# Kernel optimization log

Measured on AMD Instinct MI355X. Metric: run time of the kernel, lower is better.

## Reference

```python
import jax, jax.numpy as jnp
import numpy as np

EMBED_DIM = 1024
NUM_HEADS = 16
HEAD_DIM = EMBED_DIM // NUM_HEADS


def setup_inputs() -> dict:
    key = jax.random.key(0)
    ks = jax.random.split(key, 6)
    B, S = 2, 2048
    x = jax.random.normal(ks[0], (B, S, EMBED_DIM), dtype=jnp.float32)
    # causal boolean mask, broadcast to (B, H, S, S)
    causal = jnp.tril(jnp.ones((S, S), dtype=bool))
    mask = jnp.broadcast_to(causal, (B, NUM_HEADS, S, S))
    s_in = 1.0 / np.sqrt(EMBED_DIM)
    qkv_w = jax.random.normal(ks[1], (3 * EMBED_DIM, EMBED_DIM), dtype=jnp.float32) * s_in
    qkv_b = jax.random.normal(ks[2], (3 * EMBED_DIM,), dtype=jnp.float32) * 0.01
    proj_w = jax.random.normal(ks[3], (EMBED_DIM, EMBED_DIM), dtype=jnp.float32) * s_in
    proj_b = jax.random.normal(ks[4], (EMBED_DIM,), dtype=jnp.float32) * 0.01
    return {"x": x, "mask": mask, "qkv_w": qkv_w, "qkv_b": qkv_b,
            "proj_w": proj_w, "proj_b": proj_b}


def reference(x, mask, qkv_w, qkv_b, proj_w, proj_b):
    B, S, E = x.shape
    H, D = NUM_HEADS, HEAD_DIM
    qkv = x @ qkv_w.T + qkv_b                     # (B, S, 3E)
    q, k, v = jnp.split(qkv, 3, axis=-1)
    # (B, H, S, D)
    q = q.reshape(B, S, H, D).transpose(0, 2, 1, 3)
    k = k.reshape(B, S, H, D).transpose(0, 2, 1, 3)
    v = v.reshape(B, S, H, D).transpose(0, 2, 1, 3)
    scale = D ** (-0.5)
    attn = jnp.einsum('bhqd,bhkd->bhqk', q, k) * scale
    attn = jnp.where(mask, attn, jnp.float32(-10000.0))
    attn = attn - jnp.max(attn, axis=-1, keepdims=True)
    attn = jax.nn.softmax(attn, axis=-1)
    attn = jnp.where(mask, attn, jnp.float32(0.0))
    # dropout is identity in eval mode
    out = jnp.einsum('bhqk,bhkd->bhqd', attn, v)
    out = out.transpose(0, 2, 1, 3).reshape(B, S, E)
    return out @ proj_w.T + proj_b
```

## Files before the change

kernel.cpp:

```cpp
#include <hip/hip_runtime.h>
#include <hip/hip_bf16.h>

#define BATCH 2
#define SEQ 2048
#define EMBED 1024
#define NHEADS 16
#define HDIM 64

typedef __hip_bfloat16 bf16;
typedef __attribute__((ext_vector_type(8))) short bf16x8;
typedef __attribute__((ext_vector_type(4))) short bf16x4;
typedef __attribute__((ext_vector_type(4))) float f32x4;

typedef const __attribute__((address_space(1))) void* gaddr_t;
typedef __attribute__((address_space(3))) void* laddr_t;

__device__ __forceinline__ bf16x8 lds_frag8(const bf16* p) {
    const bf16x4 a = *(const bf16x4*)p;
    const bf16x4 b = *(const bf16x4*)(p + 4);
    return __builtin_shufflevector(a, b, 0, 1, 2, 3, 4, 5, 6, 7);
}

__global__ __launch_bounds__(256)
void f2b_kernel(const float* __restrict__ in, bf16* __restrict__ out, int n4)
{
    const int i = blockIdx.x * 256 + threadIdx.x;
    if (i >= n4) return;
    const float4 v = ((const float4*)in)[i];
    union { ushort4 u4; bf16 h[4]; } o;
    o.h[0] = __float2bfloat16(v.x);
    o.h[1] = __float2bfloat16(v.y);
    o.h[2] = __float2bfloat16(v.z);
    o.h[3] = __float2bfloat16(v.w);
    ((ushort4*)out)[i] = o.u4;
}

template<int MODE>
__global__ __launch_bounds__(256)
void gemm_bt(const bf16* __restrict__ A, const bf16* __restrict__ B,
             const float* __restrict__ bias, void* __restrict__ Cv,
             int M, int N, int K)
{
    __shared__ __align__(16) bf16 lA[128 * 32];
    __shared__ __align__(16) bf16 lB[128 * 32];
    const int tid  = threadIdx.x;
    const int bn   = blockIdx.x, bm = blockIdx.y;
    const int wave = tid >> 6, lane = tid & 63;
    const int wm   = (wave >> 1) << 6, wn = (wave & 1) << 6;
    const int quad = lane >> 4, l16 = lane & 15;

    f32x4 acc[4][4] = {};

    for (int kt = 0; kt < K; kt += 32) {
        __syncthreads();
        #pragma unroll
        for (int i = 0; i < 2; ++i) {
            const int c = tid + (i << 8);
            const int r = c >> 2, kc = (c & 3) << 3;
            const bf16* gA = A + (long)(bm * 128 + r) * K + (kt + kc);
            const bf16* gB = B + (long)(bn * 128 + r) * K + (kt + kc);
            __builtin_amdgcn_global_load_lds((gaddr_t)gA, (laddr_t)&lA[c << 3], 16, 0, 0);
            __builtin_amdgcn_global_load_lds((gaddr_t)gB, (laddr_t)&lB[c << 3], 16, 0, 0);
        }
        __syncthreads();

        bf16x8 af[4], bfr[4];
        #pragma unroll
        for (int t = 0; t < 4; ++t) {
            af[t]  = *(const bf16x8*)&lA[(wm + t * 16 + l16) * 32 + quad * 8];
            bfr[t] = *(const bf16x8*)&lB[(wn + t * 16 + l16) * 32 + quad * 8];
        }
        #pragma unroll
        for (int tm = 0; tm < 4; ++tm)
            #pragma unroll
            for (int tn = 0; tn < 4; ++tn)
                acc[tm][tn] = __builtin_amdgcn_mfma_f32_16x16x32_bf16(
                    af[tm], bfr[tn], acc[tm][tn], 0, 0, 0);
    }

    #pragma unroll
    for (int tm = 0; tm < 4; ++tm) {
        #pragma unroll
        for (int tn = 0; tn < 4; ++tn) {
            const int gn = bn * 128 + wn + tn * 16 + l16;
            const float bv = bias[gn];
            #pragma unroll
            for (int r = 0; r < 4; ++r) {
                const int gm = bm * 128 + wm + tm * 16 + quad * 4 + r;
                const float v = acc[tm][tn][r] + bv;
                if (MODE == 0) {
                    ((float*)Cv)[(long)gm * N + gn] = v;
                } else {
                    const int b = gm >> 11, s = gm & (SEQ - 1);
                    const int part = gn >> 10, h = (gn >> 6) & (NHEADS - 1), d = gn & (HDIM - 1);
                    const long off = ((((long)part * BATCH + b) * NHEADS + h) * SEQ + s) * HDIM + d;
                    ((bf16*)Cv)[off] = __float2bfloat16(v);
                }
            }
        }
    }
}

__global__ __launch_bounds__(256)
void attn_mfma(const bf16* __restrict__ Q, const bf16* __restrict__ K,
               const bf16* __restrict__ V, bf16* __restrict__ O)
{
    __shared__ __align__(16) bf16 kS[64 * 68];
    __shared__ __align__(16) bf16 vS[64 * 68];
    __shared__ __align__(16) bf16 pS[4 * 32 * 68];

    const int tid  = threadIdx.x;
    const int wave = tid >> 6, lane = tid & 63;
    const int quad = lane >> 4, l15 = lane & 15;
    const int qt   = (gridDim.x - 1) - blockIdx.x;
    const int bh   = blockIdx.y;
    const int q0   = qt * 128, qw0 = q0 + wave * 32;

    const bf16* Qb = Q + (long)bh * SEQ * HDIM;
    const bf16* Kb = K + (long)bh * SEQ * HDIM;
    const bf16* Vb = V + (long)bh * SEQ * HDIM;
    const short* vSs = (const short*)vS;
    bf16* pW = pS + wave * 32 * 68;

    bf16x8 qf[2][2];
    #pragma unroll
    for (int mt = 0; mt < 2; ++mt)
        #pragma unroll
        for (int c = 0; c < 2; ++c) {
            union { int4 i; bf16x8 v; } u;
            u.i = *(const int4*)(Qb + (long)(qw0 + mt * 16 + l15) * HDIM + c * 32 + quad * 8);
            qf[mt][c] = u.v;
        }

    f32x4 acc[2][4] = {};
    float lsum[8] = {};

    const int nkt = 2 * qt + 2;
    const float sc = 0.125f * 1.44269504088896340736f;

    for (int t = 0; t < nkt; ++t) {
        const int kb = t * 64;
        __syncthreads();
        #pragma unroll
        for (int i = 0; i < 2; ++i) {
            const int c = tid + (i << 8);
            const int row = c >> 3, col = (c & 7) << 3;
            const int4 kk = *(const int4*)(Kb + (long)(kb + row) * HDIM + col);
            const int4 vv = *(const int4*)(Vb + (long)(kb + row) * HDIM + col);
            *(int2*)&kS[row * 68 + col]     = make_int2(kk.x, kk.y);
            *(int2*)&kS[row * 68 + col + 4] = make_int2(kk.z, kk.w);
            *(int2*)&vS[row * 68 + col]     = make_int2(vv.x, vv.y);
            *(int2*)&vS[row * 68 + col + 4] = make_int2(vv.z, vv.w);
        }
        __syncthreads();
        if (kb > qw0 + 31) continue;

        f32x4 s[2][4] = {};
        #pragma unroll
        for (int c = 0; c < 2; ++c) {
            bf16x8 kf[4];
            #pragma unroll
            for (int nt = 0; nt < 4; ++nt)
                kf[nt] = lds_frag8(&kS[(nt * 16 + l15) * 68 + c * 32 + quad * 8]);
            #pragma unroll
            for (int mt = 0; mt < 2; ++mt)
                #pragma unroll
                for (int nt = 0; nt < 4; ++nt)
                    s[mt][nt] = __builtin_amdgcn_mfma_f32_16x16x32_bf16(
                        qf[mt][c], kf[nt], s[mt][nt], 0, 0, 0);
        }

        #pragma unroll
        for (int mt = 0; mt < 2; ++mt)
            #pragma unroll
            for (int nt = 0; nt < 4; ++nt)
                #pragma unroll
                for (int r = 0; r < 4; ++r) {
                    const int rl = mt * 16 + quad * 4 + r;
                    const int cl = nt * 16 + l15;
                    const float p = ((kb + cl) <= (qw0 + rl))
                        ? __builtin_amdgcn_exp2f(s[mt][nt][r] * sc) : 0.f;
                    lsum[mt * 4 + r] += p;
                    pW[rl * 68 + cl] = __float2bfloat16(p);
                }

        #pragma unroll
        for (int c = 0; c < 2; ++c) {
            bf16x8 pf[2];
            #pragma unroll
            for (int mt = 0; mt < 2; ++mt)
                pf[mt] = lds_frag8(&pW[(mt * 16 + l15) * 68 + c * 32 + quad * 8]);
            #pragma unroll
            for (int nt = 0; nt < 4; ++nt) {
                bf16x8 vf;
                #pragma unroll
                for (int j = 0; j < 8; ++j)
                    vf[j] = vSs[(c * 32 + quad * 8 + j) * 68 + nt * 16 + l15];
                #pragma unroll
                for (int mt = 0; mt < 2; ++mt)
                    acc[mt][nt] = __builtin_amdgcn_mfma_f32_16x16x32_bf16(
                        pf[mt], vf, acc[mt][nt], 0, 0, 0);
            }
        }
    }

    #pragma unroll
    for (int i = 0; i < 8; ++i) {
        #pragma unroll
        for (int m = 1; m < 16; m <<= 1) lsum[i] += __shfl_xor(lsum[i], m, 64);
        lsum[i] = 1.f / lsum[i];
    }

    const int b = bh >> 4, h = bh & 15;
    #pragma unroll
    for (int mt = 0; mt < 2; ++mt)
        #pragma unroll
        for (int r = 0; r < 4; ++r) {
            const int rl = mt * 16 + quad * 4 + r;
            bf16* orow = O + ((long)b * SEQ + (qw0 + rl)) * EMBED + h * HDIM;
            const float inv = lsum[mt * 4 + r];
            #pragma unroll
            for (int nt = 0; nt < 4; ++nt)
                orow[nt * 16 + l15] = __float2bfloat16(acc[mt][nt][r] * inv);
        }
}

extern "C" void kernel_launch(void* const* d_in, const int* in_sizes, int n_in,
                              void* d_out, int out_size, void* d_ws, size_t ws_size,
                              hipStream_t stream)
{
    const float* x      = (const float*)d_in[0];
    const float* qkv_w  = (const float*)d_in[2];
    const float* qkv_b  = (const float*)d_in[3];
    const float* proj_w = (const float*)d_in[4];
    const float* proj_b = (const float*)d_in[5];
    float* out = (float*)d_out;

    const long nX  = (long)BATCH * SEQ * EMBED;
    const long nQW = 3L * EMBED * EMBED;
    const long nPW = (long)EMBED * EMBED;
    const long per = (long)BATCH * NHEADS * SEQ * HDIM;

    bf16* xw  = (bf16*)d_ws;
    bf16* qwm = xw + nX;
    bf16* pwm = qwm + nQW;
    bf16* qw  = pwm + nPW;
    bf16* kw  = qw + per;
    bf16* vw  = kw + per;
    bf16* att = vw + per;

    f2b_kernel<<<(int)(nX  / 4 / 256), 256, 0, stream>>>(x,      xw,  (int)(nX  / 4));
    f2b_kernel<<<(int)(nQW / 4 / 256), 256, 0, stream>>>(qkv_w,  qwm, (int)(nQW / 4));
    f2b_kernel<<<(int)(nPW / 4 / 256), 256, 0, stream>>>(proj_w, pwm, (int)(nPW / 4));

    gemm_bt<1><<<dim3(3 * EMBED / 128, BATCH * SEQ / 128), 256, 0, stream>>>(
        xw, qwm, qkv_b, qw, BATCH * SEQ, 3 * EMBED, EMBED);

    attn_mfma<<<dim3(SEQ / 128, BATCH * NHEADS), 256, 0, stream>>>(qw, kw, vw, att);

    gemm_bt<0><<<dim3(EMBED / 128, BATCH * SEQ / 128), 256, 0, stream>>>(
        att, pwm, proj_b, out, BATCH * SEQ, EMBED, EMBED);
}
```

Baseline: 756.0 us.

## Split attention KV range across two blocks and combine partials; fuse conversions

The attention kernel now splits each query tile's key tiles into even and odd halves handled by separate blocks. Each block writes unnormalized fp32 partial outputs and row sums, and a new combine kernel adds the two halves, normalizes, and writes bf16. The change doubles the number of attention blocks on the GPU (512 to 1024). Because no running max is used, the halves can be summed directly. The three fp32-to-bf16 conversion launches are merged into one, and the V tile in LDS is padded to a stride of 70 to change bank access patterns. In exchange it adds fp32 partial-output traffic (about 33 MB written and read) and one extra launch.

```diff
diff --git a/kernel.cpp b/kernel.cpp
--- a/kernel.cpp
+++ b/kernel.cpp
@@ -22,17 +22,23 @@
 }
 
 __global__ __launch_bounds__(256)
-void f2b_kernel(const float* __restrict__ in, bf16* __restrict__ out, int n4)
-{
-    const int i = blockIdx.x * 256 + threadIdx.x;
-    if (i >= n4) return;
-    const float4 v = ((const float4*)in)[i];
+void f2b_all(const float* __restrict__ s0, bf16* __restrict__ d0, int n0,
+             const float* __restrict__ s1, bf16* __restrict__ d1, int n1,
+             const float* __restrict__ s2, bf16* __restrict__ d2, int n2)
+{
+    int i = blockIdx.x * 256 + threadIdx.x;
+    const float* s; bf16* d;
+    if (i < n0)                { s = s0; d = d0; }
+    else if ((i -= n0) < n1)   { s = s1; d = d1; }
+    else if ((i -= n1) < n2)   { s = s2; d = d2; }
+    else return;
+    const float4 v = ((const float4*)s)[i];
     union { ushort4 u4; bf16 h[4]; } o;
     o.h[0] = __float2bfloat16(v.x);
     o.h[1] = __float2bfloat16(v.y);
     o.h[2] = __float2bfloat16(v.z);
     o.h[3] = __float2bfloat16(v.w);
-    ((ushort4*)out)[i] = o.u4;
+    ((ushort4*)d)[i] = o.u4;
 }
 
 template<int MODE>
@@ -102,17 +108,19 @@
 }
 
 __global__ __launch_bounds__(256)
-void attn_mfma(const bf16* __restrict__ Q, const bf16* __restrict__ K,
-               const bf16* __restrict__ V, bf16* __restrict__ O)
+void attn_part(const bf16* __restrict__ Q, const bf16* __restrict__ K,
+               const bf16* __restrict__ V, float* __restrict__ Op,
+               float* __restrict__ lp)
 {
     __shared__ __align__(16) bf16 kS[64 * 68];
-    __shared__ __align__(16) bf16 vS[64 * 68];
+    __shared__ __align__(16) bf16 vS[64 * 70];
     __shared__ __align__(16) bf16 pS[4 * 32 * 68];
 
     const int tid  = threadIdx.x;
     const int wave = tid >> 6, lane = tid & 63;
     const int quad = lane >> 4, l15 = lane & 15;
-    const int qt   = (gridDim.x - 1) - blockIdx.x;
+    const int qt   = 15 - (blockIdx.x >> 1);
+    const int half = blockIdx.x & 1;
     const int bh   = blockIdx.y;
     const int q0   = qt * 128, qw0 = q0 + wave * 32;
 
@@ -122,6 +130,8 @@
     const short* vSs = (const short*)vS;
     bf16* pW = pS + wave * 32 * 68;
 
+    const int srow0 = tid >> 3, scol = (tid & 7) << 3;
+
     bf16x8 qf[2][2];
     #pragma unroll
     for (int mt = 0; mt < 2; ++mt)
@@ -135,22 +145,21 @@
     f32x4 acc[2][4] = {};
     float lsum[8] = {};
 
-    const int nkt = 2 * qt + 2;
+    const int ntile = qt + 1;
     const float sc = 0.125f * 1.44269504088896340736f;
 
-    for (int t = 0; t < nkt; ++t) {
-        const int kb = t * 64;
+    for (int j = 0; j < ntile; ++j) {
+        const int kb = (2 * j + half) * 64;
         __syncthreads();
         #pragma unroll
         for (int i = 0; i < 2; ++i) {
-            const int c = tid + (i << 8);
-            const int row = c >> 3, col = (c & 7) << 3;
-            const int4 kk = *(const int4*)(Kb + (long)(kb + row) * HDIM + col);
-            const int4 vv = *(const int4*)(Vb + (long)(kb + row) * HDIM + col);
-            *(int2*)&kS[row * 68 + col]     = make_int2(kk.x, kk.y);
-            *(int2*)&kS[row * 68 + col + 4] = make_int2(kk.z, kk.w);
-            *(int2*)&vS[row * 68 + col]     = make_int2(vv.x, vv.y);
-            *(int2*)&vS[row * 68 + col + 4] = make_int2(vv.z, vv.w);
+            const int row = srow0 + 32 * i;
+            const int4 kk = *(const int4*)(Kb + (long)(kb + row) * HDIM + scol);
+            const int4 vv = *(const int4*)(Vb + (long)(kb + row) * HDIM + scol);
+            *(int2*)&kS[row * 68 + scol]     = make_int2(kk.x, kk.y);
+            *(int2*)&kS[row * 68 + scol + 4] = make_int2(kk.z, kk.w);
+            int* vp = (int*)&vS[row * 70 + scol];
+            vp[0] = vv.x; vp[1] = vv.y; vp[2] = vv.z; vp[3] = vv.w;
         }
         __syncthreads();
         if (kb > qw0 + 31) continue;
@@ -194,8 +203,8 @@
             for (int nt = 0; nt < 4; ++nt) {
                 bf16x8 vf;
                 #pragma unroll
-                for (int j = 0; j < 8; ++j)
-                    vf[j] = vSs[(c * 32 + quad * 8 + j) * 68 + nt * 16 + l15];
+                for (int jj = 0; jj < 8; ++jj)
+                    vf[jj] = vSs[(c * 32 + quad * 8 + jj) * 70 + nt * 16 + l15];
                 #pragma unroll
                 for (int mt = 0; mt < 2; ++mt)
                     acc[mt][nt] = __builtin_amdgcn_mfma_f32_16x16x32_bf16(
@@ -205,24 +214,45 @@
     }
 
     #pragma unroll
-    for (int i = 0; i < 8; ++i) {
+    for (int i = 0; i < 8; ++i)
         #pragma unroll
         for (int m = 1; m < 16; m <<= 1) lsum[i] += __shfl_xor(lsum[i], m, 64);
-        lsum[i] = 1.f / lsum[i];
-    }
-
-    const int b = bh >> 4, h = bh & 15;
+
+    const long halfO = (long)BATCH * NHEADS * SEQ * HDIM;
+    float* Oh = Op + half * halfO + ((long)bh * SEQ) * HDIM;
+    float* lh = lp + half * (BATCH * NHEADS * SEQ) + bh * SEQ;
     #pragma unroll
     for (int mt = 0; mt < 2; ++mt)
         #pragma unroll
         for (int r = 0; r < 4; ++r) {
             const int rl = mt * 16 + quad * 4 + r;
-            bf16* orow = O + ((long)b * SEQ + (qw0 + rl)) * EMBED + h * HDIM;
-            const float inv = lsum[mt * 4 + r];
+            float* orow = Oh + (long)(qw0 + rl) * HDIM;
             #pragma unroll
             for (int nt = 0; nt < 4; ++nt)
-                orow[nt * 16 + l15] = __float2bfloat16(acc[mt][nt][r] * inv);
-        }
+                orow[nt * 16 + l15] = acc[mt][nt][r];
+            if (l15 == 0) lh[qw0 + rl] = lsum[mt * 4 + r];
+        }
+}
+
+__global__ __launch_bounds__(256)
+void attn_combine(const float* __restrict__ Op, const float* __restrict__ lp,
+                  bf16* __restrict__ att)
+{
+    const int i = blockIdx.x * 256 + threadIdx.x;
+    const int d4 = i & 15, q = (i >> 4) & (SEQ - 1), bh = i >> 15;
+    const long halfO = (long)BATCH * NHEADS * SEQ * HDIM;
+    const long rowo  = ((long)bh * SEQ + q) * HDIM;
+    const float4 a = ((const float4*)(Op + rowo))[d4];
+    const float4 b = ((const float4*)(Op + halfO + rowo))[d4];
+    const int li = bh * SEQ + q;
+    const float inv = 1.f / (lp[li] + lp[BATCH * NHEADS * SEQ + li]);
+    const int bb = bh >> 4, h = bh & 15;
+    union { ushort4 u4; bf16 hv[4]; } o;
+    o.hv[0] = __float2bfloat16((a.x + b.x) * inv);
+    o.hv[1] = __float2bfloat16((a.y + b.y) * inv);
+    o.hv[2] = __float2bfloat16((a.z + b.z) * inv);
+    o.hv[3] = __float2bfloat16((a.w + b.w) * inv);
+    *(ushort4*)(att + ((long)bb * SEQ + q) * EMBED + h * HDIM + d4 * 4) = o.u4;
 }
 
 extern "C" void kernel_launch(void* const* d_in, const int* in_sizes, int n_in,
@@ -248,15 +278,19 @@
     bf16* kw  = qw + per;
     bf16* vw  = kw + per;
     bf16* att = vw + per;
-
-    f2b_kernel<<<(int)(nX  / 4 / 256), 256, 0, stream>>>(x,      xw,  (int)(nX  / 4));
-    f2b_kernel<<<(int)(nQW / 4 / 256), 256, 0, stream>>>(qkv_w,  qwm, (int)(nQW / 4));
-    f2b_kernel<<<(int)(nPW / 4 / 256), 256, 0, stream>>>(proj_w, pwm, (int)(nPW / 4));
+    float* Op = (float*)(att + per);
+    float* lp = Op + 2 * per;
+
+    const int n0 = (int)(nX / 4), n1 = (int)(nQW / 4), n2 = (int)(nPW / 4);
+    f2b_all<<<(n0 + n1 + n2 + 255) / 256, 256, 0, stream>>>(
+        x, xw, n0, qkv_w, qwm, n1, proj_w, pwm, n2);
 
     gemm_bt<1><<<dim3(3 * EMBED / 128, BATCH * SEQ / 128), 256, 0, stream>>>(
         xw, qwm, qkv_b, qw, BATCH * SEQ, 3 * EMBED, EMBED);
 
-    attn_mfma<<<dim3(SEQ / 128, BATCH * NHEADS), 256, 0, stream>>>(qw, kw, vw, att);
+    attn_part<<<dim3(2 * SEQ / 128, BATCH * NHEADS), 256, 0, stream>>>(
+        qw, kw, vw, Op, lp);
+    attn_combine<<<(int)(per / 4 / 256), 256, 0, stream>>>(Op, lp, att);
 
     gemm_bt<0><<<dim3(EMBED / 128, BATCH * SEQ / 128), 256, 0, stream>>>(
         att, pwm, proj_b, out, BATCH * SEQ, EMBED, EMBED);
```

Result: no change. 756.2 us (+0.0%).

## Store V transposed and load K/V fragments directly from global in attention

Applied to the files above, without the earlier changes.

The QKV GEMM epilogue now writes V in a transposed [d][seq] layout with packed 4-element stores. The attention kernel drops the shared-memory K/V staging and its block barriers, and each wave reads K and V^T MFMA fragments straight from global/L2 with 16-byte loads. Each wave also runs only the key tiles its own query rows need, so waves in a block no longer wait on each other. The three fp32-to-bf16 conversion launches are merged into one. The cost is that K/V reuse across the four waves now comes from cache instead of LDS, which adds global traffic and latency.

```diff
diff --git a/kernel.cpp b/kernel.cpp
--- a/kernel.cpp
+++ b/kernel.cpp
@@ -22,17 +22,23 @@
 }
 
 __global__ __launch_bounds__(256)
-void f2b_kernel(const float* __restrict__ in, bf16* __restrict__ out, int n4)
-{
-    const int i = blockIdx.x * 256 + threadIdx.x;
-    if (i >= n4) return;
-    const float4 v = ((const float4*)in)[i];
+void f2b_all(const float* __restrict__ s0, bf16* __restrict__ d0, int n0,
+             const float* __restrict__ s1, bf16* __restrict__ d1, int n1,
+             const float* __restrict__ s2, bf16* __restrict__ d2, int n2)
+{
+    int i = blockIdx.x * 256 + threadIdx.x;
+    const float* s; bf16* d;
+    if (i < n0)                { s = s0; d = d0; }
+    else if ((i -= n0) < n1)   { s = s1; d = d1; }
+    else if ((i -= n1) < n2)   { s = s2; d = d2; }
+    else return;
+    const float4 v = ((const float4*)s)[i];
     union { ushort4 u4; bf16 h[4]; } o;
     o.h[0] = __float2bfloat16(v.x);
     o.h[1] = __float2bfloat16(v.y);
     o.h[2] = __float2bfloat16(v.z);
     o.h[3] = __float2bfloat16(v.w);
-    ((ushort4*)out)[i] = o.u4;
+    ((ushort4*)d)[i] = o.u4;
 }
 
 template<int MODE>
@@ -84,17 +90,28 @@
         for (int tn = 0; tn < 4; ++tn) {
             const int gn = bn * 128 + wn + tn * 16 + l16;
             const float bv = bias[gn];
-            #pragma unroll
-            for (int r = 0; r < 4; ++r) {
-                const int gm = bm * 128 + wm + tm * 16 + quad * 4 + r;
-                const float v = acc[tm][tn][r] + bv;
-                if (MODE == 0) {
-                    ((float*)Cv)[(long)gm * N + gn] = v;
+            if (MODE == 0) {
+                #pragma unroll
+                for (int r = 0; r < 4; ++r) {
+                    const int gm = bm * 128 + wm + tm * 16 + quad * 4 + r;
+                    ((float*)Cv)[(long)gm * N + gn] = acc[tm][tn][r] + bv;
+                }
+            } else {
+                const int part = gn >> 10, h = (gn >> 6) & (NHEADS - 1), d = gn & (HDIM - 1);
+                const int gm0 = bm * 128 + wm + tm * 16 + quad * 4;
+                const int b = gm0 >> 11, s0 = gm0 & (SEQ - 1);
+                if (part == 2) {
+                    union { ushort4 u4; bf16 hv[4]; } o;
+                    #pragma unroll
+                    for (int r = 0; r < 4; ++r) o.hv[r] = __float2bfloat16(acc[tm][tn][r] + bv);
+                    const long off = ((((long)2 * BATCH + b) * NHEADS + h) * HDIM + d) * SEQ + s0;
+                    *(ushort4*)((bf16*)Cv + off) = o.u4;
                 } else {
-                    const int b = gm >> 11, s = gm & (SEQ - 1);
-                    const int part = gn >> 10, h = (gn >> 6) & (NHEADS - 1), d = gn & (HDIM - 1);
-                    const long off = ((((long)part * BATCH + b) * NHEADS + h) * SEQ + s) * HDIM + d;
-                    ((bf16*)Cv)[off] = __float2bfloat16(v);
+                    #pragma unroll
+                    for (int r = 0; r < 4; ++r) {
+                        const long off = ((((long)part * BATCH + b) * NHEADS + h) * SEQ + (s0 + r)) * HDIM + d;
+                        ((bf16*)Cv)[off] = __float2bfloat16(acc[tm][tn][r] + bv);
+                    }
                 }
             }
         }
@@ -102,24 +119,21 @@
 }
 
 __global__ __launch_bounds__(256)
-void attn_mfma(const bf16* __restrict__ Q, const bf16* __restrict__ K,
-               const bf16* __restrict__ V, bf16* __restrict__ O)
-{
-    __shared__ __align__(16) bf16 kS[64 * 68];
-    __shared__ __align__(16) bf16 vS[64 * 68];
+void attn_nf(const bf16* __restrict__ Q, const bf16* __restrict__ K,
+             const bf16* __restrict__ Vt, bf16* __restrict__ O)
+{
     __shared__ __align__(16) bf16 pS[4 * 32 * 68];
 
     const int tid  = threadIdx.x;
     const int wave = tid >> 6, lane = tid & 63;
     const int quad = lane >> 4, l15 = lane & 15;
-    const int qt   = (gridDim.x - 1) - blockIdx.x;
     const int bh   = blockIdx.y;
-    const int q0   = qt * 128, qw0 = q0 + wave * 32;
-
-    const bf16* Qb = Q + (long)bh * SEQ * HDIM;
-    const bf16* Kb = K + (long)bh * SEQ * HDIM;
-    const bf16* Vb = V + (long)bh * SEQ * HDIM;
-    const short* vSs = (const short*)vS;
+    const int qg   = (15 - blockIdx.x) * 4 + wave;
+    const int qw0  = qg * 32;
+
+    const bf16* Qb  = Q  + (long)bh * SEQ * HDIM;
+    const bf16* Kb  = K  + (long)bh * SEQ * HDIM;
+    const bf16* Vtb = Vt + (long)bh * HDIM * SEQ;
     bf16* pW = pS + wave * 32 * 68;
 
     bf16x8 qf[2][2];
@@ -135,39 +149,24 @@
     f32x4 acc[2][4] = {};
     float lsum[8] = {};
 
-    const int nkt = 2 * qt + 2;
+    const int nkt = (qw0 >> 6) + 1;
     const float sc = 0.125f * 1.44269504088896340736f;
 
     for (int t = 0; t < nkt; ++t) {
         const int kb = t * 64;
-        __syncthreads();
-        #pragma unroll
-        for (int i = 0; i < 2; ++i) {
-            const int c = tid + (i << 8);
-            const int row = c >> 3, col = (c & 7) << 3;
-            const int4 kk = *(const int4*)(Kb + (long)(kb + row) * HDIM + col);
-            const int4 vv = *(const int4*)(Vb + (long)(kb + row) * HDIM + col);
-            *(int2*)&kS[row * 68 + col]     = make_int2(kk.x, kk.y);
-            *(int2*)&kS[row * 68 + col + 4] = make_int2(kk.z, kk.w);
-            *(int2*)&vS[row * 68 + col]     = make_int2(vv.x, vv.y);
-            *(int2*)&vS[row * 68 + col + 4] = make_int2(vv.z, vv.w);
-        }
-        __syncthreads();
-        if (kb > qw0 + 31) continue;
 
         f32x4 s[2][4] = {};
         #pragma unroll
         for (int c = 0; c < 2; ++c) {
-            bf16x8 kf[4];
-            #pragma unroll
-            for (int nt = 0; nt < 4; ++nt)
-                kf[nt] = lds_frag8(&kS[(nt * 16 + l15) * 68 + c * 32 + quad * 8]);
-            #pragma unroll
-            for (int mt = 0; mt < 2; ++mt)
-                #pragma unroll
-                for (int nt = 0; nt < 4; ++nt)
+            #pragma unroll
+            for (int nt = 0; nt < 4; ++nt) {
+                union { int4 i; bf16x8 v; } u;
+                u.i = *(const int4*)(Kb + (long)(kb + nt * 16 + l15) * HDIM + c * 32 + quad * 8);
+                #pragma unroll
+                for (int mt = 0; mt < 2; ++mt)
                     s[mt][nt] = __builtin_amdgcn_mfma_f32_16x16x32_bf16(
-                        qf[mt][c], kf[nt], s[mt][nt], 0, 0, 0);
+                        qf[mt][c], u.v, s[mt][nt], 0, 0, 0);
+            }
         }
 
         #pragma unroll
@@ -192,14 +191,12 @@
                 pf[mt] = lds_frag8(&pW[(mt * 16 + l15) * 68 + c * 32 + quad * 8]);
             #pragma unroll
             for (int nt = 0; nt < 4; ++nt) {
-                bf16x8 vf;
-                #pragma unroll
-                for (int j = 0; j < 8; ++j)
-                    vf[j] = vSs[(c * 32 + quad * 8 + j) * 68 + nt * 16 + l15];
+                union { int4 i; bf16x8 v; } u;
+                u.i = *(const int4*)(Vtb + (long)(nt * 16 + l15) * SEQ + kb + c * 32 + quad * 8);
                 #pragma unroll
                 for (int mt = 0; mt < 2; ++mt)
                     acc[mt][nt] = __builtin_amdgcn_mfma_f32_16x16x32_bf16(
-                        pf[mt], vf, acc[mt][nt], 0, 0, 0);
+                        pf[mt], u.v, acc[mt][nt], 0, 0, 0);
             }
         }
     }
@@ -249,14 +246,14 @@
     bf16* vw  = kw + per;
     bf16* att = vw + per;
 
-    f2b_kernel<<<(int)(nX  / 4 / 256), 256, 0, stream>>>(x,      xw,  (int)(nX  / 4));
-    f2b_kernel<<<(int)(nQW / 4 / 256), 256, 0, stream>>>(qkv_w,  qwm, (int)(nQW / 4));
-    f2b_kernel<<<(int)(nPW / 4 / 256), 256, 0, stream>>>(proj_w, pwm, (int)(nPW / 4));
+    const int n0 = (int)(nX / 4), n1 = (int)(nQW / 4), n2 = (int)(nPW / 4);
+    f2b_all<<<(n0 + n1 + n2 + 255) / 256, 256, 0, stream>>>(
+        x, xw, n0, qkv_w, qwm, n1, proj_w, pwm, n2);
 
     gemm_bt<1><<<dim3(3 * EMBED / 128, BATCH * SEQ / 128), 256, 0, stream>>>(
         xw, qwm, qkv_b, qw, BATCH * SEQ, 3 * EMBED, EMBED);
 
-    attn_mfma<<<dim3(SEQ / 128, BATCH * NHEADS), 256, 0, stream>>>(qw, kw, vw, att);
+    attn_nf<<<dim3(16, BATCH * NHEADS), 256, 0, stream>>>(qw, kw, vw, att);
 
     gemm_bt<0><<<dim3(EMBED / 128, BATCH * SEQ / 128), 256, 0, stream>>>(
         att, pwm, proj_b, out, BATCH * SEQ, EMBED, EMBED);
```

Measured after the change: 765.9 us. Within noise of the previous version (+1.3%).
